# Kernel optimization log

Hardware: AMD Instinct MI355X
Metric: run time of the kernel (lower is better)

Reference implementation:

```python
import jax, jax.numpy as jnp
import numpy as np

NEG_INF = -9e15
ALPHA = 0.2  # LeakyReLU negative slope

N = 8192
D_IN = 512
D_OUT = 256


def setup_inputs() -> dict:
    key = jax.random.key(0)
    k1, k2, k3, k4, k5 = jax.random.split(key, 5)
    features = jax.random.normal(k1, (N, D_IN), dtype=jnp.float32)
    adjacency_matrix = jax.random.randint(k2, (N, N), 0, 2, dtype=jnp.int32)
    # learned params (torch Linear stores [out, in]; we use [in, out] layout)
    s_phi = 1.0 / np.sqrt(D_IN)
    W_phi = jax.random.uniform(k3, (D_IN, D_OUT), jnp.float32, -s_phi, s_phi)
    s_v = 1.0 / np.sqrt(D_OUT)
    w_mu = jax.random.uniform(k4, (D_OUT,), jnp.float32, -s_v, s_v)
    w_xi = jax.random.uniform(k5, (D_OUT,), jnp.float32, -s_v, s_v)
    return {"features": features, "adjacency_matrix": adjacency_matrix,
            "W_phi": W_phi, "w_mu": w_mu, "w_xi": w_xi}


def reference(features, adjacency_matrix, W_phi, w_mu, w_xi):
    h = features @ W_phi                                   # [N, d_out]
    mu = h @ w_mu                                          # [N]
    xi = h @ w_xi                                          # [N]
    e = mu[:, None] + xi[None, :]                          # [N, N] additive scores
    e = jnp.where(e >= 0, e, ALPHA * e)                    # LeakyReLU
    e = jnp.where(adjacency_matrix > 0, e, NEG_INF)        # mask non-edges
    a = jax.nn.softmax(e, axis=1)                          # row softmax (dropout p=0)
    out = a @ h                                            # weighted aggregation
    return jax.nn.elu(out)
```

## Files before the change

kernel.cpp:

```cpp
#include <hip/hip_runtime.h>
#include <cstdint>
#include <cstddef>


#define LOG2E 1.44269504f

typedef __attribute__((ext_vector_type(8))) short short8;
typedef __attribute__((ext_vector_type(4))) float floatx4;

using uint_as1 = __attribute__((address_space(1))) unsigned int;
using uint_as3 = __attribute__((address_space(3))) unsigned int;

__device__ __forceinline__ void gld_lds16(const void* g, void* l) {
  __builtin_amdgcn_global_load_lds((const uint_as1*)g, (uint_as3*)l, 16, 0, 0);
}

__device__ __forceinline__ unsigned short f2b(float f) {
  unsigned u = __float_as_uint(f);
  u += 0x7fffu + ((u >> 16) & 1u);
  return (unsigned short)(u >> 16);
}
__device__ __forceinline__ float b2f(short s) {
  return __uint_as_float(((unsigned)(unsigned short)s) << 16);
}

__device__ __forceinline__ unsigned cvtpk_bf16(float a, float b) {
  unsigned r;
  asm("v_cvt_pk_bf16_f32 %0, %1, %2" : "=v"(r) : "v"(a), "v"(b));
  return r;
}

__global__ void k_cvt_features(const float* __restrict__ f, unsigned short* __restrict__ fb) {
  int tid = blockIdx.x * 256 + threadIdx.x;
  float4 v = ((const float4*)f)[tid];
  ushort4 o = {f2b(v.x), f2b(v.y), f2b(v.z), f2b(v.w)};
  *(ushort4*)&fb[tid * 4] = o;
}

__global__ void k_prep_wt(const float* __restrict__ w, unsigned short* __restrict__ wt) {
  int tid = blockIdx.x * 256 + threadIdx.x;
  int n = tid >> 9, k = tid & 511;
  wt[n * 512 + k] = f2b(w[k * 256 + n]);
}

__global__ void k_prep_p(const float* __restrict__ w, const float* __restrict__ wmu,
                         const float* __restrict__ wxi, float* __restrict__ pmu,
                         float* __restrict__ pxi) {
  int tid = blockIdx.x * 256 + threadIdx.x;
  int k = tid >> 2, seg = tid & 3;
  float sm = 0.f, sx = 0.f;
  int base = k * 256 + seg * 64;
#pragma unroll
  for (int c = 0; c < 64; c += 4) {
    float4 wv = *(const float4*)&w[base + c];
    float4 mv = *(const float4*)&wmu[seg * 64 + c];
    float4 xv = *(const float4*)&wxi[seg * 64 + c];
    sm += wv.x * mv.x + wv.y * mv.y + wv.z * mv.z + wv.w * mv.w;
    sx += wv.x * xv.x + wv.y * xv.y + wv.z * xv.z + wv.w * xv.w;
  }
  sm += __shfl_xor(sm, 1); sm += __shfl_xor(sm, 2);
  sx += __shfl_xor(sx, 1); sx += __shfl_xor(sx, 2);
  if (seg == 0) { pmu[k] = sm; pxi[k] = sx; }
}

__global__ void k_mu_xi(const unsigned short* __restrict__ fb, const float* __restrict__ pmu,
                        const float* __restrict__ pxi, float* __restrict__ Emu,
                        float* __restrict__ Fmu, float* __restrict__ Exi,
                        float* __restrict__ Fxi) {
  int w = threadIdx.x >> 6, l = threadIdx.x & 63;
  int i = blockIdx.x * 4 + w;
  short8 fv = *(const short8*)&fb[i * 512 + l * 8];
  float m = 0.f, x = 0.f;
#pragma unroll
  for (int c = 0; c < 8; ++c) {
    float fvf = b2f(fv[c]);
    m = fmaf(fvf, pmu[l * 8 + c], m);
    x = fmaf(fvf, pxi[l * 8 + c], x);
  }
#pragma unroll
  for (int off = 32; off > 0; off >>= 1) {
    m += __shfl_xor(m, off);
    x += __shfl_xor(x, off);
  }
  if (l == 0) {
    float ms = m * LOG2E, xs = x * LOG2E;
    Emu[i] = __builtin_amdgcn_exp2f(ms);
    Fmu[i] = __builtin_amdgcn_exp2f(0.2f * ms);
    Exi[i] = __builtin_amdgcn_exp2f(xs);
    Fxi[i] = __builtin_amdgcn_exp2f(0.2f * xs);
  }
}

__global__ __launch_bounds__(256, 2) void k_gemm1(const unsigned short* __restrict__ fb,
                                                  const unsigned short* __restrict__ wt,
                                                  unsigned short* __restrict__ ht) {
  __shared__ __align__(16) unsigned short As[64 * 64];
  __shared__ __align__(16) unsigned short Bs[128 * 64];
  int t = threadIdx.x, w = t >> 6, l = t & 63;
  int bm_ = blockIdx.x >> 1, bn = blockIdx.x & 1;
  int m0 = bm_ * 64, n0 = bn * 128;
  int lr = l >> 3, lg = l & 7, g = lg ^ lr;
  int kg = l >> 4, ln = l & 15;
  floatx4 zero = {0.f, 0.f, 0.f, 0.f};
  floatx4 acc[4][2];
#pragma unroll
  for (int mf = 0; mf < 4; ++mf)
#pragma unroll
    for (int nf = 0; nf < 2; ++nf) acc[mf][nf] = zero;

  for (int it = 0; it < 8; ++it) {
    int k0 = it * 64;
#pragma unroll
    for (int q = 0; q < 2; ++q) {
      int row = w * 16 + q * 8 + lr;
      const void* gp = fb + (size_t)(m0 + row) * 512 + k0 + g * 8;
      int lb = __builtin_amdgcn_readfirstlane((w * 16 + q * 8) * 64);
      gld_lds16(gp, &As[lb]);
    }
#pragma unroll
    for (int q = 0; q < 4; ++q) {
      int row = w * 32 + q * 8 + lr;
      const void* gp = wt + (size_t)(n0 + row) * 512 + k0 + g * 8;
      int lb = __builtin_amdgcn_readfirstlane((w * 32 + q * 8) * 64);
      gld_lds16(gp, &Bs[lb]);
    }
    __syncthreads();
#pragma unroll
    for (int ks = 0; ks < 2; ++ks) {
      int gg = ks * 4 + kg;
      int swz = (gg ^ (ln & 7)) * 8;
      short8 bfr[2];
#pragma unroll
      for (int nf = 0; nf < 2; ++nf)
        bfr[nf] = *(const short8*)&Bs[(w * 32 + nf * 16 + ln) * 64 + swz];
#pragma unroll
      for (int mf = 0; mf < 4; ++mf) {
        short8 afr = *(const short8*)&As[(mf * 16 + ln) * 64 + swz];
#pragma unroll
        for (int nf = 0; nf < 2; ++nf)
          acc[mf][nf] = __builtin_amdgcn_mfma_f32_16x16x32_bf16(afr, bfr[nf], acc[mf][nf], 0, 0, 0);
      }
    }
    __syncthreads();
  }
#pragma unroll
  for (int mf = 0; mf < 4; ++mf)
#pragma unroll
    for (int nf = 0; nf < 2; ++nf) {
      int ng = n0 + w * 32 + nf * 16 + ln;
      int mg = m0 + mf * 16 + kg * 4;
      ushort4 o = {f2b(acc[mf][nf][0]), f2b(acc[mf][nf][1]),
                   f2b(acc[mf][nf][2]), f2b(acc[mf][nf][3])};
      *(ushort4*)&ht[(size_t)ng * 8192 + mg] = o;
    }
}

__global__ __launch_bounds__(512, 2) void k_gatt9(const int* __restrict__ adjm,
                                                  const unsigned short* __restrict__ ht,
                                                  const float* __restrict__ Emu,
                                                  const float* __restrict__ Fmu,
                                                  const float* __restrict__ Exi,
                                                  const float* __restrict__ Fxi,
                                                  float* __restrict__ nump,
                                                  float* __restrict__ zpart) {
  __shared__ __align__(16) unsigned short Bs[2][256 * 32];
  __shared__ __align__(16) int Aj[2][256 * 32];
  __shared__ __align__(16) float EfE[1024];
  __shared__ __align__(16) float EfF[1024];

  int t = threadIdx.x, w = t >> 6, l = t & 63;
  int ln = l & 15, kg = l >> 4;
  int jb = blockIdx.x & 7, ig = blockIdx.x >> 3;
  int i0 = ig * 256;
  int jc0 = jb * 1024;

  if (t < 256) {
    *(float4*)&EfE[t * 4] = *(const float4*)&Exi[jc0 + t * 4];
  } else {
    int t2 = t - 256;
    *(float4*)&EfF[t2 * 4] = *(const float4*)&Fxi[jc0 + t2 * 4];
  }

  float EM[2], FM[2];
#pragma unroll
  for (int mf = 0; mf < 2; ++mf) {
    int i = i0 + w * 32 + mf * 16 + ln;
    EM[mf] = Emu[i];
    FM[mf] = Fmu[i];
  }

  floatx4 zero = {0.f, 0.f, 0.f, 0.f};
  floatx4 acc[2][16];
#pragma unroll
  for (int mf = 0; mf < 2; ++mf)
#pragma unroll
    for (int nf = 0; nf < 16; ++nf) acc[mf][nf] = zero;
  float zacc[2] = {0.f, 0.f};

#define STAGE_B(win_, b_)                                                   \
  {                                                                         \
    int j0_ = jc0 + (win_) * 32;                                            \
    _Pragma("unroll")                                                       \
    for (int q = 0; q < 2; ++q) {                                           \
      int rowbase = w * 32 + q * 16;                                        \
      int row = rowbase + (l >> 2);                                         \
      int g = (l & 3) ^ ((row >> 1) & 3);                                   \
      const void* gp = ht + (size_t)row * 8192 + j0_ + g * 8;               \
      int lb = __builtin_amdgcn_readfirstlane((b_) * (256 * 32) + rowbase * 32); \
      gld_lds16(gp, &((unsigned short*)Bs)[lb]);                            \
    }                                                                       \
  }

#define STAGE_A(win_, b_)                                                   \
  {                                                                         \
    int j0_ = jc0 + (win_) * 32;                                            \
    _Pragma("unroll")                                                       \
    for (int q = 0; q < 4; ++q) {                                           \
      int rowbase = w * 32 + q * 8;                                         \
      int rr = l >> 3;                                                      \
      int row = rowbase + rr;                                               \
      int wslot = (l & 7) ^ rr;                                             \
      const void* gp = adjm + (size_t)(i0 + row) * 8192 + j0_ + wslot * 4;  \
      int lb = __builtin_amdgcn_readfirstlane((b_) * (256 * 32) + rowbase * 32); \
      gld_lds16(gp, &((int*)Aj)[lb]);                                       \
    }                                                                       \
  }

  STAGE_B(0, 0);
  STAGE_A(0, 0);
  __syncthreads();

  for (int win = 0; win < 32; ++win) {
    int buf = win & 1;
    if (win < 31) {
      STAGE_B(win + 1, buf ^ 1);
      STAGE_A(win + 1, buf ^ 1);
    }
    int jl = win * 32 + kg * 8;
    float4 e0 = *(const float4*)&EfE[jl];
    float4 e1 = *(const float4*)&EfE[jl + 4];
    float4 f0 = *(const float4*)&EfF[jl];
    float4 f1 = *(const float4*)&EfF[jl + 4];
    float ex[8] = {e0.x, e0.y, e0.z, e0.w, e1.x, e1.y, e1.z, e1.w};
    float fx[8] = {f0.x, f0.y, f0.z, f0.w, f1.x, f1.y, f1.z, f1.w};
    short8 af[2];
#pragma unroll
    for (int mf = 0; mf < 2; ++mf) {
      int i_loc = w * 32 + mf * 16 + ln;
      int rr = ln & 7;
      const int* arow = &((const int*)Aj)[buf * (256 * 32) + i_loc * 32];
      int4 a0 = *(const int4*)&arow[((2 * kg) ^ rr) * 4];
      int4 a1 = *(const int4*)&arow[((2 * kg + 1) ^ rr) * 4];
      int av[8] = {a0.x, a0.y, a0.z, a0.w, a1.x, a1.y, a1.z, a1.w};
      float A = EM[mf], F = FM[mf];
      union { unsigned u[4]; short8 s; } cv;
      float zs = 0.f;
#pragma unroll
      for (int p = 0; p < 4; ++p) {
        float m0 = fmaxf(A * ex[2 * p], F * fx[2 * p]);
        float m1 = fmaxf(A * ex[2 * p + 1], F * fx[2 * p + 1]);
        m0 = (av[2 * p] != 0) ? m0 : 0.f;
        m1 = (av[2 * p + 1] != 0) ? m1 : 0.f;
        zs += m0;
        zs += m1;
        cv.u[p] = cvtpk_bf16(m0, m1);
      }
      zacc[mf] += zs;
      af[mf] = cv.s;
    }
#pragma unroll
    for (int half = 0; half < 2; ++half) {
      short8 bfv[8];
#pragma unroll
      for (int nf = 0; nf < 8; ++nf) {
        int n = half * 128 + nf * 16 + ln;
        bfv[nf] = *(const short8*)&Bs[buf][n * 32 + ((kg ^ ((n >> 1) & 3)) * 8)];
      }
#pragma unroll
      for (int mf = 0; mf < 2; ++mf)
#pragma unroll
        for (int nf = 0; nf < 8; ++nf)
          acc[mf][half * 8 + nf] = __builtin_amdgcn_mfma_f32_16x16x32_bf16(
              af[mf], bfv[nf], acc[mf][half * 8 + nf], 0, 0, 0);
    }
    __syncthreads();
  }
#undef STAGE_B
#undef STAGE_A

#pragma unroll
  for (int mf = 0; mf < 2; ++mf) {
    float z = zacc[mf];
    z += __shfl_xor(z, 16);
    z += __shfl_xor(z, 32);
    if (l < 16) zpart[(size_t)jb * 8192 + i0 + w * 32 + mf * 16 + ln] = z;
  }

  float* np = nump + (size_t)jb * (8192 * 256);
#pragma unroll
  for (int mf = 0; mf < 2; ++mf) {
    int rowb = i0 + w * 32 + mf * 16 + kg * 4;
#pragma unroll
    for (int r = 0; r < 4; ++r) {
      float* rp = np + (size_t)(rowb + r) * 256;
#pragma unroll
      for (int nf = 0; nf < 16; ++nf)
        rp[nf * 16 + ln] = acc[mf][nf][r];
    }
  }
}

__global__ void k_final(const float* __restrict__ nump, const float* __restrict__ zpart,
                        float* __restrict__ out) {
  int tid = blockIdx.x * 256 + threadIdx.x;
  int i = tid >> 6;
  float z = 0.f;
#pragma unroll
  for (int p = 0; p < 8; ++p) z += zpart[(size_t)p * 8192 + i];
  float zi = 1.0f / z;
  float4 v = {0.f, 0.f, 0.f, 0.f};
#pragma unroll
  for (int p = 0; p < 8; ++p) {
    float4 s = *(const float4*)&nump[(size_t)p * (8192 * 256) + tid * 4];
    v.x += s.x; v.y += s.y; v.z += s.z; v.w += s.w;
  }
  v.x *= zi; v.y *= zi; v.z *= zi; v.w *= zi;
  v.x = (v.x > 0.f) ? v.x : (__builtin_amdgcn_exp2f(v.x * LOG2E) - 1.f);
  v.y = (v.y > 0.f) ? v.y : (__builtin_amdgcn_exp2f(v.y * LOG2E) - 1.f);
  v.z = (v.z > 0.f) ? v.z : (__builtin_amdgcn_exp2f(v.z * LOG2E) - 1.f);
  v.w = (v.w > 0.f) ? v.w : (__builtin_amdgcn_exp2f(v.w * LOG2E) - 1.f);
  *(float4*)&out[tid * 4] = v;
}

extern "C" void kernel_launch(void* const* d_in, const int* in_sizes, int n_in,
                              void* d_out, int out_size, void* d_ws, size_t ws_size,
                              hipStream_t stream) {
  const float* features = (const float*)d_in[0];
  const int* adjm = (const int*)d_in[1];
  const float* W_phi = (const float*)d_in[2];
  const float* w_mu = (const float*)d_in[3];
  const float* w_xi = (const float*)d_in[4];
  float* out = (float*)d_out;

  char* ws = (char*)d_ws;
  unsigned short* fb  = (unsigned short*)(ws + 0);
  unsigned short* ht  = (unsigned short*)(ws + 8388608);
  unsigned short* wt  = (unsigned short*)(ws + 12582912);
  float* pmu = (float*)(ws + 12845056);
  float* pxi = (float*)(ws + 12847104);
  float* Emu = (float*)(ws + 12849152);
  float* Fmu = (float*)(ws + 12881920);
  float* Exi = (float*)(ws + 12914688);
  float* Fxi = (float*)(ws + 12947456);
  float* zpart = (float*)(ws + 12980224);
  float* nump = (float*)(ws + 25165824);

  k_cvt_features<<<4096, 256, 0, stream>>>(features, fb);
  k_prep_wt<<<512, 256, 0, stream>>>(W_phi, wt);
  k_prep_p<<<8, 256, 0, stream>>>(W_phi, w_mu, w_xi, pmu, pxi);
  k_mu_xi<<<2048, 256, 0, stream>>>(fb, pmu, pxi, Emu, Fmu, Exi, Fxi);
  k_gemm1<<<256, 256, 0, stream>>>(fb, wt, ht);
  k_gatt9<<<256, 512, 0, stream>>>(adjm, ht, Emu, Fmu, Exi, Fxi, nump, zpart);
  k_final<<<2048, 256, 0, stream>>>(nump, zpart, out);
}
```

Baseline: 449.0 us.

## Split-K within block, reduce partials in LDS and fuse normalization epilogue

The attention kernel now gives each block 32 rows and splits the 8192-column reduction across its 8 waves. Each wave reads adjacency and ht directly from global memory with no LDS staging or per-window barriers. Partial accumulators and row sums are combined through a tree reduction in shared memory, and the final 1/z scaling and ELU are applied in-kernel. This removes the 64 MB partial-numerator write, its read-back, and the separate final kernel. In exchange, the main loop relies on uncoalesced 16-byte global loads of ht with no software pipelining, and the reduction serializes through several barriers with one wave writing all output.

```diff
diff --git a/kernel.cpp b/kernel.cpp
--- a/kernel.cpp
+++ b/kernel.cpp
@@ -155,39 +155,39 @@
     }
 }
 
-__global__ __launch_bounds__(512, 2) void k_gatt9(const int* __restrict__ adjm,
-                                                  const unsigned short* __restrict__ ht,
-                                                  const float* __restrict__ Emu,
-                                                  const float* __restrict__ Fmu,
-                                                  const float* __restrict__ Exi,
-                                                  const float* __restrict__ Fxi,
-                                                  float* __restrict__ nump,
-                                                  float* __restrict__ zpart) {
-  __shared__ __align__(16) unsigned short Bs[2][256 * 32];
-  __shared__ __align__(16) int Aj[2][256 * 32];
-  __shared__ __align__(16) float EfE[1024];
-  __shared__ __align__(16) float EfF[1024];
+__global__ __launch_bounds__(512, 2) void k_gatt11(const int* __restrict__ adjm,
+                                                   const unsigned short* __restrict__ ht,
+                                                   const float* __restrict__ Emu,
+                                                   const float* __restrict__ Fmu,
+                                                   const float* __restrict__ Exi,
+                                                   const float* __restrict__ Fxi,
+                                                   float* __restrict__ out) {
+  __shared__ __align__(16) char smem[131072];
+  __shared__ __align__(16) float zb[8][32];
+  __shared__ float zinv_s[32];
+
+  float* EfE = (float*)smem;
+  float* EfF = (float*)(smem + 32768);
 
   int t = threadIdx.x, w = t >> 6, l = t & 63;
   int ln = l & 15, kg = l >> 4;
-  int jb = blockIdx.x & 7, ig = blockIdx.x >> 3;
-  int i0 = ig * 256;
-  int jc0 = jb * 1024;
-
-  if (t < 256) {
-    *(float4*)&EfE[t * 4] = *(const float4*)&Exi[jc0 + t * 4];
-  } else {
-    int t2 = t - 256;
-    *(float4*)&EfF[t2 * 4] = *(const float4*)&Fxi[jc0 + t2 * 4];
-  }
-
+  int i0 = blockIdx.x * 32;
+  int jw0 = w * 1024;
+
+#pragma unroll
+  for (int q = 0; q < 4; ++q) {
+    int idx = q * 2048 + t * 4;
+    *(float4*)&EfE[idx] = *(const float4*)&Exi[idx];
+    *(float4*)&EfF[idx] = *(const float4*)&Fxi[idx];
+  }
   float EM[2], FM[2];
 #pragma unroll
   for (int mf = 0; mf < 2; ++mf) {
-    int i = i0 + w * 32 + mf * 16 + ln;
+    int i = i0 + mf * 16 + ln;
     EM[mf] = Emu[i];
     FM[mf] = Fmu[i];
   }
+  __syncthreads();
 
   floatx4 zero = {0.f, 0.f, 0.f, 0.f};
   floatx4 acc[2][16];
@@ -197,61 +197,28 @@
     for (int nf = 0; nf < 16; ++nf) acc[mf][nf] = zero;
   float zacc[2] = {0.f, 0.f};
 
-#define STAGE_B(win_, b_)                                                   \
-  {                                                                         \
-    int j0_ = jc0 + (win_) * 32;                                            \
-    _Pragma("unroll")                                                       \
-    for (int q = 0; q < 2; ++q) {                                           \
-      int rowbase = w * 32 + q * 16;                                        \
-      int row = rowbase + (l >> 2);                                         \
-      int g = (l & 3) ^ ((row >> 1) & 3);                                   \
-      const void* gp = ht + (size_t)row * 8192 + j0_ + g * 8;               \
-      int lb = __builtin_amdgcn_readfirstlane((b_) * (256 * 32) + rowbase * 32); \
-      gld_lds16(gp, &((unsigned short*)Bs)[lb]);                            \
-    }                                                                       \
-  }
-
-#define STAGE_A(win_, b_)                                                   \
-  {                                                                         \
-    int j0_ = jc0 + (win_) * 32;                                            \
-    _Pragma("unroll")                                                       \
-    for (int q = 0; q < 4; ++q) {                                           \
-      int rowbase = w * 32 + q * 8;                                         \
-      int rr = l >> 3;                                                      \
-      int row = rowbase + rr;                                               \
-      int wslot = (l & 7) ^ rr;                                             \
-      const void* gp = adjm + (size_t)(i0 + row) * 8192 + j0_ + wslot * 4;  \
-      int lb = __builtin_amdgcn_readfirstlane((b_) * (256 * 32) + rowbase * 32); \
-      gld_lds16(gp, &((int*)Aj)[lb]);                                       \
-    }                                                                       \
-  }
-
-  STAGE_B(0, 0);
-  STAGE_A(0, 0);
-  __syncthreads();
-
-  for (int win = 0; win < 32; ++win) {
-    int buf = win & 1;
-    if (win < 31) {
-      STAGE_B(win + 1, buf ^ 1);
-      STAGE_A(win + 1, buf ^ 1);
-    }
-    int jl = win * 32 + kg * 8;
-    float4 e0 = *(const float4*)&EfE[jl];
-    float4 e1 = *(const float4*)&EfE[jl + 4];
-    float4 f0 = *(const float4*)&EfF[jl];
-    float4 f1 = *(const float4*)&EfF[jl + 4];
+  const int* arow0 = adjm + (size_t)(i0 + ln) * 8192 + jw0 + kg * 8;
+  const int* arow1 = arow0 + (size_t)16 * 8192;
+
+#pragma unroll 2
+  for (int ks = 0; ks < 32; ++ks) {
+    int j = jw0 + ks * 32 + kg * 8;
+    int4 a00 = *(const int4*)(arow0 + ks * 32);
+    int4 a01 = *(const int4*)(arow0 + ks * 32 + 4);
+    int4 a10 = *(const int4*)(arow1 + ks * 32);
+    int4 a11 = *(const int4*)(arow1 + ks * 32 + 4);
+    float4 e0 = *(const float4*)&EfE[j];
+    float4 e1 = *(const float4*)&EfE[j + 4];
+    float4 f0 = *(const float4*)&EfF[j];
+    float4 f1 = *(const float4*)&EfF[j + 4];
     float ex[8] = {e0.x, e0.y, e0.z, e0.w, e1.x, e1.y, e1.z, e1.w};
     float fx[8] = {f0.x, f0.y, f0.z, f0.w, f1.x, f1.y, f1.z, f1.w};
+    int av0[8] = {a00.x, a00.y, a00.z, a00.w, a01.x, a01.y, a01.z, a01.w};
+    int av1[8] = {a10.x, a10.y, a10.z, a10.w, a11.x, a11.y, a11.z, a11.w};
     short8 af[2];
 #pragma unroll
     for (int mf = 0; mf < 2; ++mf) {
-      int i_loc = w * 32 + mf * 16 + ln;
-      int rr = ln & 7;
-      const int* arow = &((const int*)Aj)[buf * (256 * 32) + i_loc * 32];
-      int4 a0 = *(const int4*)&arow[((2 * kg) ^ rr) * 4];
-      int4 a1 = *(const int4*)&arow[((2 * kg + 1) ^ rr) * 4];
-      int av[8] = {a0.x, a0.y, a0.z, a0.w, a1.x, a1.y, a1.z, a1.w};
+      const int* av = (mf == 0) ? av0 : av1;
       float A = EM[mf], F = FM[mf];
       union { unsigned u[4]; short8 s; } cv;
       float zs = 0.f;
@@ -272,64 +239,79 @@
     for (int half = 0; half < 2; ++half) {
       short8 bfv[8];
 #pragma unroll
-      for (int nf = 0; nf < 8; ++nf) {
-        int n = half * 128 + nf * 16 + ln;
-        bfv[nf] = *(const short8*)&Bs[buf][n * 32 + ((kg ^ ((n >> 1) & 3)) * 8)];
+      for (int nf2 = 0; nf2 < 8; ++nf2) {
+        int n = half * 128 + nf2 * 16 + ln;
+        bfv[nf2] = *(const short8*)&ht[(size_t)n * 8192 + j];
       }
 #pragma unroll
       for (int mf = 0; mf < 2; ++mf)
 #pragma unroll
-        for (int nf = 0; nf < 8; ++nf)
-          acc[mf][half * 8 + nf] = __builtin_amdgcn_mfma_f32_16x16x32_bf16(
-              af[mf], bfv[nf], acc[mf][half * 8 + nf], 0, 0, 0);
-    }
-    __syncthreads();
-  }
-#undef STAGE_B
-#undef STAGE_A
+        for (int nf2 = 0; nf2 < 8; ++nf2)
+          acc[mf][half * 8 + nf2] = __builtin_amdgcn_mfma_f32_16x16x32_bf16(
+              af[mf], bfv[nf2], acc[mf][half * 8 + nf2], 0, 0, 0);
+    }
+  }
 
 #pragma unroll
   for (int mf = 0; mf < 2; ++mf) {
     float z = zacc[mf];
     z += __shfl_xor(z, 16);
     z += __shfl_xor(z, 32);
-    if (l < 16) zpart[(size_t)jb * 8192 + i0 + w * 32 + mf * 16 + ln] = z;
-  }
-
-  float* np = nump + (size_t)jb * (8192 * 256);
-#pragma unroll
-  for (int mf = 0; mf < 2; ++mf) {
-    int rowb = i0 + w * 32 + mf * 16 + kg * 4;
-#pragma unroll
-    for (int r = 0; r < 4; ++r) {
-      float* rp = np + (size_t)(rowb + r) * 256;
+    if (l < 16) zb[w][mf * 16 + l] = z;
+  }
+  __syncthreads();
+  if (t < 32) {
+    float z = 0.f;
+#pragma unroll
+    for (int p = 0; p < 8; ++p) z += zb[p][t];
+    zinv_s[t] = 1.0f / z;
+  }
+
+  float* red = (float*)smem;
+#define RED_W(slot_)                                                        \
+  {                                                                         \
+    float* dst = red + (slot_) * 8192;                                      \
+    _Pragma("unroll")                                                       \
+    for (int mf = 0; mf < 2; ++mf)                                          \
+      _Pragma("unroll")                                                     \
+      for (int nf = 0; nf < 16; ++nf)                                       \
+        *(floatx4*)&dst[(mf * 16 + nf) * 256 + l * 4] = acc[mf][nf];        \
+  }
+#define RED_R(slot_)                                                        \
+  {                                                                         \
+    const float* src = red + (slot_) * 8192;                                \
+    _Pragma("unroll")                                                       \
+    for (int mf = 0; mf < 2; ++mf)                                          \
+      _Pragma("unroll")                                                     \
+      for (int nf = 0; nf < 16; ++nf)                                       \
+        acc[mf][nf] += *(const floatx4*)&src[(mf * 16 + nf) * 256 + l * 4]; \
+  }
+  if (w >= 4) RED_W(w - 4);
+  __syncthreads();
+  if (w < 4) RED_R(w);
+  __syncthreads();
+  if (w == 2 || w == 3) RED_W(w - 2);
+  __syncthreads();
+  if (w < 2) RED_R(w);
+  __syncthreads();
+  if (w == 1) RED_W(0);
+  __syncthreads();
+  if (w == 0) {
+    RED_R(0);
+#pragma unroll
+    for (int mf = 0; mf < 2; ++mf)
 #pragma unroll
       for (int nf = 0; nf < 16; ++nf)
-        rp[nf * 16 + ln] = acc[mf][nf][r];
-    }
-  }
-}
-
-__global__ void k_final(const float* __restrict__ nump, const float* __restrict__ zpart,
-                        float* __restrict__ out) {
-  int tid = blockIdx.x * 256 + threadIdx.x;
-  int i = tid >> 6;
-  float z = 0.f;
-#pragma unroll
-  for (int p = 0; p < 8; ++p) z += zpart[(size_t)p * 8192 + i];
-  float zi = 1.0f / z;
-  float4 v = {0.f, 0.f, 0.f, 0.f};
-#pragma unroll
-  for (int p = 0; p < 8; ++p) {
-    float4 s = *(const float4*)&nump[(size_t)p * (8192 * 256) + tid * 4];
-    v.x += s.x; v.y += s.y; v.z += s.z; v.w += s.w;
-  }
-  v.x *= zi; v.y *= zi; v.z *= zi; v.w *= zi;
-  v.x = (v.x > 0.f) ? v.x : (__builtin_amdgcn_exp2f(v.x * LOG2E) - 1.f);
-  v.y = (v.y > 0.f) ? v.y : (__builtin_amdgcn_exp2f(v.y * LOG2E) - 1.f);
-  v.z = (v.z > 0.f) ? v.z : (__builtin_amdgcn_exp2f(v.z * LOG2E) - 1.f);
-  v.w = (v.w > 0.f) ? v.w : (__builtin_amdgcn_exp2f(v.w * LOG2E) - 1.f);
-  *(float4*)&out[tid * 4] = v;
+#pragma unroll
+        for (int r = 0; r < 4; ++r) {
+          int row = mf * 16 + kg * 4 + r;
+          float val = acc[mf][nf][r] * zinv_s[row];
+          val = (val > 0.f) ? val : (__builtin_amdgcn_exp2f(val * LOG2E) - 1.f);
+          out[(size_t)(i0 + row) * 256 + nf * 16 + ln] = val;
+        }
+  }
+#undef RED_W
+#undef RED_R
 }
 
 extern "C" void kernel_launch(void* const* d_in, const int* in_sizes, int n_in,
@@ -352,14 +334,11 @@
   float* Fmu = (float*)(ws + 12881920);
   float* Exi = (float*)(ws + 12914688);
   float* Fxi = (float*)(ws + 12947456);
-  float* zpart = (float*)(ws + 12980224);
-  float* nump = (float*)(ws + 25165824);
 
   k_cvt_features<<<4096, 256, 0, stream>>>(features, fb);
   k_prep_wt<<<512, 256, 0, stream>>>(W_phi, wt);
   k_prep_p<<<8, 256, 0, stream>>>(W_phi, w_mu, w_xi, pmu, pxi);
   k_mu_xi<<<2048, 256, 0, stream>>>(fb, pmu, pxi, Emu, Fmu, Exi, Fxi);
   k_gemm1<<<256, 256, 0, stream>>>(fb, wt, ht);
-  k_gatt9<<<256, 512, 0, stream>>>(adjm, ht, Emu, Fmu, Exi, Fxi, nump, zpart);
-  k_final<<<2048, 256, 0, stream>>>(nump, zpart, out);
-}
+  k_gatt11<<<256, 512, 0, stream>>>(adjm, ht, Emu, Fmu, Exi, Fxi, out);
+}
```

After: 516.2 us. 14.9% more time.

## Load adjacency straight into registers and deepen B-tile pipeline to four buffers

Applied to the files above, without the earlier changes.

The attention kernel now reads adjacency tiles directly from global memory into registers, one window ahead, instead of staging them through LDS. The ht (B) tiles move to a four-slot LDS ring with a prefetch distance of two. The end-of-loop __syncthreads is replaced by an explicit vmcnt wait plus s_barrier at the top of each iteration. This frees LDS and removes the LDS round trip for the mask, and should hide global latency better. The risks are more register pressure, lane-strided global loads for the adjacency, and fragile hand-written waitcnt ordering; launch bounds also drop to one block per CU.

```diff
diff --git a/kernel.cpp b/kernel.cpp
--- a/kernel.cpp
+++ b/kernel.cpp
@@ -155,16 +155,15 @@
     }
 }
 
-__global__ __launch_bounds__(512, 2) void k_gatt9(const int* __restrict__ adjm,
-                                                  const unsigned short* __restrict__ ht,
-                                                  const float* __restrict__ Emu,
-                                                  const float* __restrict__ Fmu,
-                                                  const float* __restrict__ Exi,
-                                                  const float* __restrict__ Fxi,
-                                                  float* __restrict__ nump,
-                                                  float* __restrict__ zpart) {
-  __shared__ __align__(16) unsigned short Bs[2][256 * 32];
-  __shared__ __align__(16) int Aj[2][256 * 32];
+__global__ __launch_bounds__(512, 1) void k_gatt12(const int* __restrict__ adjm,
+                                                   const unsigned short* __restrict__ ht,
+                                                   const float* __restrict__ Emu,
+                                                   const float* __restrict__ Fmu,
+                                                   const float* __restrict__ Exi,
+                                                   const float* __restrict__ Fxi,
+                                                   float* __restrict__ nump,
+                                                   float* __restrict__ zpart) {
+  __shared__ __align__(16) unsigned short Bs[4][256 * 32];
   __shared__ __align__(16) float EfE[1024];
   __shared__ __align__(16) float EfF[1024];
 
@@ -188,6 +187,9 @@
     EM[mf] = Emu[i];
     FM[mf] = Fmu[i];
   }
+
+  const int* ar0 = adjm + (size_t)(i0 + w * 32 + ln) * 8192 + jc0 + kg * 8;
+  const int* ar1 = ar0 + (size_t)16 * 8192;
 
   floatx4 zero = {0.f, 0.f, 0.f, 0.f};
   floatx4 acc[2][16];
@@ -211,31 +213,25 @@
     }                                                                       \
   }
 
-#define STAGE_A(win_, b_)                                                   \
-  {                                                                         \
-    int j0_ = jc0 + (win_) * 32;                                            \
-    _Pragma("unroll")                                                       \
-    for (int q = 0; q < 4; ++q) {                                           \
-      int rowbase = w * 32 + q * 8;                                         \
-      int rr = l >> 3;                                                      \
-      int row = rowbase + rr;                                               \
-      int wslot = (l & 7) ^ rr;                                             \
-      const void* gp = adjm + (size_t)(i0 + row) * 8192 + j0_ + wslot * 4;  \
-      int lb = __builtin_amdgcn_readfirstlane((b_) * (256 * 32) + rowbase * 32); \
-      gld_lds16(gp, &((int*)Aj)[lb]);                                       \
-    }                                                                       \
-  }
-
+  int4 acur[4], anext[4];
+  acur[0] = *(const int4*)(ar0 + 0);
+  acur[1] = *(const int4*)(ar0 + 4);
+  acur[2] = *(const int4*)(ar1 + 0);
+  acur[3] = *(const int4*)(ar1 + 4);
   STAGE_B(0, 0);
-  STAGE_A(0, 0);
+  STAGE_B(1, 1);
   __syncthreads();
 
   for (int win = 0; win < 32; ++win) {
-    int buf = win & 1;
+    int bR = win & 3;
     if (win < 31) {
-      STAGE_B(win + 1, buf ^ 1);
-      STAGE_A(win + 1, buf ^ 1);
-    }
+      asm volatile("s_waitcnt vmcnt(2)" ::: "memory");
+    } else {
+      asm volatile("s_waitcnt vmcnt(0)" ::: "memory");
+    }
+    __builtin_amdgcn_s_barrier();
+    asm volatile("" ::: "memory");
+
     int jl = win * 32 + kg * 8;
     float4 e0 = *(const float4*)&EfE[jl];
     float4 e1 = *(const float4*)&EfE[jl + 4];
@@ -246,12 +242,14 @@
     short8 af[2];
 #pragma unroll
     for (int mf = 0; mf < 2; ++mf) {
-      int i_loc = w * 32 + mf * 16 + ln;
-      int rr = ln & 7;
-      const int* arow = &((const int*)Aj)[buf * (256 * 32) + i_loc * 32];
-      int4 a0 = *(const int4*)&arow[((2 * kg) ^ rr) * 4];
-      int4 a1 = *(const int4*)&arow[((2 * kg + 1) ^ rr) * 4];
-      int av[8] = {a0.x, a0.y, a0.z, a0.w, a1.x, a1.y, a1.z, a1.w};
+      int av[8];
+      if (mf == 0) {
+        av[0] = acur[0].x; av[1] = acur[0].y; av[2] = acur[0].z; av[3] = acur[0].w;
+        av[4] = acur[1].x; av[5] = acur[1].y; av[6] = acur[1].z; av[7] = acur[1].w;
+      } else {
+        av[0] = acur[2].x; av[1] = acur[2].y; av[2] = acur[2].z; av[3] = acur[2].w;
+        av[4] = acur[3].x; av[5] = acur[3].y; av[6] = acur[3].z; av[7] = acur[3].w;
+      }
       float A = EM[mf], F = FM[mf];
       union { unsigned u[4]; short8 s; } cv;
       float zs = 0.f;
@@ -274,7 +272,7 @@
 #pragma unroll
       for (int nf = 0; nf < 8; ++nf) {
         int n = half * 128 + nf * 16 + ln;
-        bfv[nf] = *(const short8*)&Bs[buf][n * 32 + ((kg ^ ((n >> 1) & 3)) * 8)];
+        bfv[nf] = *(const short8*)&Bs[bR][n * 32 + ((kg ^ ((n >> 1) & 3)) * 8)];
       }
 #pragma unroll
       for (int mf = 0; mf < 2; ++mf)
@@ -283,10 +281,20 @@
           acc[mf][half * 8 + nf] = __builtin_amdgcn_mfma_f32_16x16x32_bf16(
               af[mf], bfv[nf], acc[mf][half * 8 + nf], 0, 0, 0);
     }
-    __syncthreads();
+    if (win < 31) {
+      int joff = (win + 1) * 32;
+      anext[0] = *(const int4*)(ar0 + joff);
+      anext[1] = *(const int4*)(ar0 + joff + 4);
+      anext[2] = *(const int4*)(ar1 + joff);
+      anext[3] = *(const int4*)(ar1 + joff + 4);
+    }
+    if (win < 30) {
+      STAGE_B(win + 2, (win + 2) & 3);
+    }
+    acur[0] = anext[0]; acur[1] = anext[1];
+    acur[2] = anext[2]; acur[3] = anext[3];
   }
 #undef STAGE_B
-#undef STAGE_A
 
 #pragma unroll
   for (int mf = 0; mf < 2; ++mf) {
@@ -360,6 +368,6 @@
   k_prep_p<<<8, 256, 0, stream>>>(W_phi, w_mu, w_xi, pmu, pxi);
   k_mu_xi<<<2048, 256, 0, stream>>>(fb, pmu, pxi, Emu, Fmu, Exi, Fxi);
   k_gemm1<<<256, 256, 0, stream>>>(fb, wt, ht);
-  k_gatt9<<<256, 512, 0, stream>>>(adjm, ht, Emu, Fmu, Exi, Fxi, nump, zpart);
+  k_gatt12<<<256, 512, 0, stream>>>(adjm, ht, Emu, Fmu, Exi, Fxi, nump, zpart);
   k_final<<<2048, 256, 0, stream>>>(nump, zpart, out);
 }
```

After: 450.1 us. No clear change (+0.2%).
